# Optimization experiments

Hardware: AMD Instinct MI355X
Metric: run time of the kernel (lower is better)

The kernel has to match this reference:

```python
import jax, jax.numpy as jnp
import numpy as np

NEG_LARGE = -2.0**32 + 1.0


def setup_inputs() -> dict:
    key = jax.random.key(0)
    ks = jax.random.split(key, 8)
    B, L, D = 2048, 200, 64  # D = embedding_dim, features are 2D wide
    H1, H2 = 80, 40
    queries = jax.random.normal(ks[0], (B, 2 * D), dtype=jnp.float32)
    user_behaviors = jax.random.normal(ks[1], (B, L, 2 * D), dtype=jnp.float32)
    masks = jax.random.randint(ks[2], (B, L), 0, 2, dtype=jnp.int32)
    s = 1.0 / np.sqrt(8 * D)
    w1 = jax.random.uniform(ks[3], (8 * D, H1), minval=-s, maxval=s, dtype=jnp.float32)
    b1 = jnp.zeros((H1,), jnp.float32)
    s2 = 1.0 / np.sqrt(H1)
    w2 = jax.random.uniform(ks[4], (H1, H2), minval=-s2, maxval=s2, dtype=jnp.float32)
    b2 = jnp.zeros((H2,), jnp.float32)
    s3 = 1.0 / np.sqrt(H2)
    w3 = jax.random.uniform(ks[5], (H2, 1), minval=-s3, maxval=s3, dtype=jnp.float32)
    b3 = jnp.zeros((1,), jnp.float32)
    return {"queries": queries, "user_behaviors": user_behaviors, "masks": masks,
            "w1": w1, "b1": b1, "w2": w2, "b2": b2, "w3": w3, "b3": b3}


def reference(queries, user_behaviors, masks, w1, b1, w2, b2, w3, b3):
    B, L, twoD = user_behaviors.shape
    q = jnp.broadcast_to(queries[:, None, :], (B, L, twoD))  # (B, L, 2D)
    feats = jnp.concatenate([q, user_behaviors, q - user_behaviors,
                             q * user_behaviors], axis=-1)  # (B, L, 8D)
    h = jax.nn.sigmoid(jnp.einsum('blf,fh->blh', feats, w1) + b1)
    h = jax.nn.sigmoid(jnp.einsum('blh,hk->blk', h, w2) + b2)
    scores = jnp.einsum('blk,ko->blo', h, w3) + b3  # (B, L, 1)
    valid = (masks != 0)[:, :, None]
    scores = jnp.where(valid, scores, NEG_LARGE)
    attn = jax.nn.softmax(scores, axis=1)  # (B, L, 1)
    return jnp.sum(attn * user_behaviors, axis=1)  # (B, 2D)
```

## Files before the change

### kernel.cpp

```cpp
#include <hip/hip_runtime.h>
#include <cstddef>


#define L_   200
#define D2_  128

typedef __attribute__((ext_vector_type(8))) short bf16x8;
typedef __attribute__((ext_vector_type(4))) float f32x4;
typedef __attribute__((ext_vector_type(4))) unsigned int u32x4;

__device__ __forceinline__ float sigmoidf_(float x) { return 1.0f / (1.0f + __expf(-x)); }

__device__ __forceinline__ unsigned int f2bf_(float x) {
  unsigned int u = __float_as_uint(x);
  return (u + 0x7fffu + ((u >> 16) & 1u)) >> 16;
}
__device__ __forceinline__ unsigned int pk2_(float a, float b) {
  return f2bf_(a) | (f2bf_(b) << 16);
}

extern "C" __global__ void __launch_bounds__(256, 3)
din_attn_kernel(const float* __restrict__ queries,
                const float* __restrict__ ub,
                const int*   __restrict__ masks,
                const float* __restrict__ w1,
                const float* __restrict__ b1,
                const float* __restrict__ w2,
                const float* __restrict__ b2,
                const float* __restrict__ w3,
                float* __restrict__ out)
{
  __shared__ __align__(16) char pool[39936];
  __shared__ __align__(16) char w2f[9216];
  __shared__ __align__(16) float q_s[128];
  __shared__ __align__(16) float qt_s[80];
  __shared__ __align__(16) float b2_s[48];
  __shared__ __align__(16) float w3_s[48];
  __shared__ __align__(16) float scores_s[208];
  __shared__ float red_s[8];

  const int b    = blockIdx.x;
  const int t    = threadIdx.x;
  const int wave = t >> 6;
  const int lane = t & 63;

  const float* ubbase = ub + (size_t)b * L_ * D2_;
  const float4* ub4base = (const float4*)ubbase;

  if (t < 128) q_s[t] = queries[(size_t)b * D2_ + t];
  if (t < 48) {
    b2_s[t] = (t < 40) ? b2[t] : 0.0f;
    w3_s[t] = (t < 40) ? w3[t] : 0.0f;
  }
  __syncthreads();

  if (t < 80) {
    float acc = b1[t];
    #pragma unroll 4
    for (int k = 0; k < 128; ++k)
      acc += q_s[k] * (w1[k * 80 + t] + w1[(256 + k) * 80 + t]);
    qt_s[t] = acc;
  }

  {
    u32x4* dst = (u32x4*)(pool + 13312);
    #pragma unroll
    for (int i = 0; i < 5; ++i) {
      int s = i * 256 + t;
      int n = s & 15, kg = (s >> 4) & 3, g = s >> 6;
      int kc = g / 5, nt = g - kc * 5;
      int h = nt * 16 + n, k0 = kc * 32 + kg * 8;
      float wv[8];
      #pragma unroll
      for (int j = 0; j < 8; ++j) {
        int k = k0 + j;
        wv[j] = w1[(128 + k) * 80 + h] - w1[(256 + k) * 80 + h]
              + q_s[k] * w1[(384 + k) * 80 + h];
      }
      u32x4 v = { pk2_(wv[0], wv[1]), pk2_(wv[2], wv[3]),
                  pk2_(wv[4], wv[5]), pk2_(wv[6], wv[7]) };
      dst[s] = v;
    }
  }

  {
    u32x4* dst = (u32x4*)w2f;
    #pragma unroll
    for (int i = 0; i < 3; ++i) {
      int s = i * 256 + t;
      if (s < 576) {
        int n = s & 15, g = s >> 4;
        int nt2 = g / 12, kg = g - nt2 * 12;
        int j = nt2 * 16 + n;
        u32x4 v = { 0u, 0u, 0u, 0u };
        if (j < 40 && kg < 10) {
          int k0 = kg * 8;
          float e0 = w2[(k0 + 0) * 40 + j], e1 = w2[(k0 + 1) * 40 + j];
          float e2 = w2[(k0 + 2) * 40 + j], e3 = w2[(k0 + 3) * 40 + j];
          float e4 = w2[(k0 + 4) * 40 + j], e5 = w2[(k0 + 5) * 40 + j];
          float e6 = w2[(k0 + 6) * 40 + j], e7 = w2[(k0 + 7) * 40 + j];
          v = (u32x4){ pk2_(e0, e1), pk2_(e2, e3), pk2_(e4, e5), pk2_(e6, e7) };
        }
        dst[s] = v;
      }
    }
  }

  f32x4 acc[17];
  #pragma unroll
  for (int i = 0; i < 17; ++i) acc[i] = (f32x4){0.f, 0.f, 0.f, 0.f};

  const bf16x8* Af = (const bf16x8*)pool;
  const bf16x8* Bf = (const bf16x8*)(pool + 13312);

  for (int kc = 0; kc < 4; ++kc) {
    u32x4* dst = (u32x4*)pool;
    #pragma unroll
    for (int i = 0; i < 4; ++i) {
      int s = i * 256 + t;
      if (s < 832) {
        int m = s & 15, kg = (s >> 4) & 3, mt = s >> 6;
        int l = mt * 16 + m;
        u32x4 v = { 0u, 0u, 0u, 0u };
        if (l < L_) {
          const float4* src = (const float4*)(ubbase + (size_t)l * D2_ + kc * 32 + kg * 8);
          float4 u0 = src[0], u1 = src[1];
          v = (u32x4){ pk2_(u0.x, u0.y), pk2_(u0.z, u0.w), pk2_(u1.x, u1.y), pk2_(u1.z, u1.w) };
        }
        dst[s] = v;
      }
    }
    __syncthreads();

    #pragma unroll
    for (int i = 0; i < 17; ++i) {
      int tt = i * 4 + wave;
      if (tt < 65) {
        int mt = tt / 5, nt = tt - mt * 5;
        bf16x8 av = Af[mt * 64 + lane];
        bf16x8 bv = Bf[(kc * 5 + nt) * 64 + lane];
        acc[i] = __builtin_amdgcn_mfma_f32_16x16x32_bf16(av, bv, acc[i], 0, 0, 0);
      }
    }
    __syncthreads();
  }

  {
    u32x4* pz = (u32x4*)pool;
    #pragma unroll
    for (int s = 0; s < 2; ++s) {
      int idx = s * 256 + t;
      if (idx < 416) {
        int mt = idx >> 5, off = idx & 31;
        pz[(mt * 12 + 10) * 16 + off] = (u32x4){ 0u, 0u, 0u, 0u };
      }
    }
    unsigned short* hv = (unsigned short*)pool;
    const int n = lane & 15, rg = lane >> 4;
    #pragma unroll
    for (int i = 0; i < 17; ++i) {
      int tt = i * 4 + wave;
      if (tt < 65) {
        int mt = tt / 5, nt = tt - mt * 5;
        int h = nt * 16 + n;
        int kg = h >> 3, hb = h & 7;
        float qtv = qt_s[h];
        #pragma unroll
        for (int r = 0; r < 4; ++r) {
          float x = acc[i][r] + qtv;
          hv[((mt * 12 + kg) * 16 + rg * 4 + r) * 8 + hb] = (unsigned short)f2bf_(sigmoidf_(x));
        }
      }
    }
  }
  __syncthreads();

  f32x4 acc2[4][3];
  #pragma unroll
  for (int i = 0; i < 4; ++i)
    #pragma unroll
    for (int n2 = 0; n2 < 3; ++n2) acc2[i][n2] = (f32x4){0.f, 0.f, 0.f, 0.f};

  {
    const bf16x8* hvf = (const bf16x8*)pool;
    const bf16x8* w2ff = (const bf16x8*)w2f;
    #pragma unroll
    for (int i = 0; i < 4; ++i) {
      int mt = wave + i * 4;
      if (mt < 13) {
        #pragma unroll
        for (int ks = 0; ks < 3; ++ks) {
          bf16x8 av = hvf[mt * 192 + ks * 64 + lane];
          #pragma unroll
          for (int n2 = 0; n2 < 3; ++n2) {
            bf16x8 bv = w2ff[n2 * 192 + ks * 64 + lane];
            acc2[i][n2] = __builtin_amdgcn_mfma_f32_16x16x32_bf16(av, bv, acc2[i][n2], 0, 0, 0);
          }
        }
      }
    }
  }

  {
    const int n = lane & 15, rg = lane >> 4;
    #pragma unroll
    for (int i = 0; i < 4; ++i) {
      int mt = wave + i * 4;
      if (mt < 13) {
        #pragma unroll
        for (int r = 0; r < 4; ++r) {
          float s = 0.0f;
          #pragma unroll
          for (int n2 = 0; n2 < 3; ++n2) {
            int j = n2 * 16 + n;
            s += sigmoidf_(acc2[i][n2][r] + b2_s[j]) * w3_s[j];
          }
          s += __shfl_xor(s, 1, 64);
          s += __shfl_xor(s, 2, 64);
          s += __shfl_xor(s, 4, 64);
          s += __shfl_xor(s, 8, 64);
          int l = mt * 16 + rg * 4 + r;
          if (n == 0 && l < L_) scores_s[l] = s;
        }
      }
    }
  }
  __syncthreads();

  float sval = -INFINITY;
  if (t < L_) {
    int mv = masks[(size_t)b * L_ + t];
    sval = mv ? scores_s[t] : -4294967295.0f;
  }
  float m = sval;
  #pragma unroll
  for (int o = 32; o > 0; o >>= 1) m = fmaxf(m, __shfl_xor(m, o, 64));
  if (lane == 0) red_s[wave] = m;
  __syncthreads();
  m = fmaxf(fmaxf(red_s[0], red_s[1]), fmaxf(red_s[2], red_s[3]));
  float e = (t < L_) ? __expf(sval - m) : 0.0f;
  float ssum = e;
  #pragma unroll
  for (int o = 32; o > 0; o >>= 1) ssum += __shfl_xor(ssum, o, 64);
  if (lane == 0) red_s[4 + wave] = ssum;
  __syncthreads();
  ssum = red_s[4] + red_s[5] + red_s[6] + red_s[7];
  float attn = e / ssum;
  __syncthreads();
  if (t < L_) scores_s[t] = attn;
  __syncthreads();

  {
    float* wsum = (float*)pool;
    int d4 = t & 31;
    int lg = t >> 5;
    float4 o = make_float4(0.f, 0.f, 0.f, 0.f);
    #pragma unroll 5
    for (int l = lg; l < L_; l += 8) {
      float w = scores_s[l];
      float4 v = ub4base[l * 32 + d4];
      o.x += w * v.x; o.y += w * v.y; o.z += w * v.z; o.w += w * v.w;
    }
    *(float4*)(wsum + lg * 136 + d4 * 4) = o;
    __syncthreads();
    if (t < 128) {
      float s = 0.0f;
      #pragma unroll
      for (int g = 0; g < 8; ++g) s += wsum[g * 136 + t];
      out[(size_t)b * 128 + t] = s;
    }
  }
}

extern "C" void kernel_launch(void* const* d_in, const int* in_sizes, int n_in,
                              void* d_out, int out_size, void* d_ws, size_t ws_size,
                              hipStream_t stream) {
  const float* queries = (const float*)d_in[0];
  const float* ub      = (const float*)d_in[1];
  const int*   masks   = (const int*)d_in[2];
  const float* w1      = (const float*)d_in[3];
  const float* b1      = (const float*)d_in[4];
  const float* w2      = (const float*)d_in[5];
  const float* b2      = (const float*)d_in[6];
  const float* w3      = (const float*)d_in[7];
  float* out = (float*)d_out;

  const int B = in_sizes[0] / D2_;
  din_attn_kernel<<<B, 256, 0, stream>>>(queries, ub, masks, w1, b1, w2, b2, w3, out);
}
```

Baseline: 391.0 us.

## Split weight prep into setup kernel and load MFMA A operands directly from global

Moves the per-batch qt projection and the batch-invariant W1/W2 re-layout into a separate setup kernel that writes to workspace. The main kernel then only combines precomputed wbc + q*wd, and w2 fragments are read from global memory. Behavior rows are now loaded straight into registers as MFMA A operands, so the per-chunk LDS staging and its barriers go away, and the B fragments are kept in registers. Together with the smaller LDS footprint this allows 4 blocks per CU. The cost is an extra kernel launch, uncoalesced per-lane global loads for the A operands, and global reads of w2 fragments.

```diff
diff --git a/kernel.cpp b/kernel.cpp
--- a/kernel.cpp
+++ b/kernel.cpp
@@ -9,6 +9,8 @@
 typedef __attribute__((ext_vector_type(4))) float f32x4;
 typedef __attribute__((ext_vector_type(4))) unsigned int u32x4;
 
+union U8 { u32x4 u; bf16x8 b; };
+
 __device__ __forceinline__ float sigmoidf_(float x) { return 1.0f / (1.0f + __expf(-x)); }
 
 __device__ __forceinline__ unsigned int f2bf_(float x) {
@@ -19,20 +21,89 @@
   return f2bf_(a) | (f2bf_(b) << 16);
 }
 
-extern "C" __global__ void __launch_bounds__(256, 3)
+extern "C" __global__ void __launch_bounds__(128)
+din_setup_kernel(const float* __restrict__ queries,
+                 const float* __restrict__ w1,
+                 const float* __restrict__ b1,
+                 const float* __restrict__ w2,
+                 float* __restrict__ qt,
+                 float* __restrict__ wbc,
+                 float* __restrict__ wd,
+                 u32x4* __restrict__ w2a,
+                 u32x4* __restrict__ w2b)
+{
+  const int bb = blockIdx.x;
+  const int t  = threadIdx.x;
+
+  if (bb < 8) {
+    for (int s = bb * 160 + t; s < bb * 160 + 160; s += 128) {
+      int nn = s & 15, kg = (s >> 4) & 3, g = s >> 6;
+      int kc = g / 5, nt = g - kc * 5;
+      int h = nt * 16 + nn, k0 = kc * 32 + kg * 8;
+      #pragma unroll
+      for (int j = 0; j < 8; ++j) {
+        int k = k0 + j;
+        wbc[s * 8 + j] = w1[(128 + k) * 80 + h] - w1[(256 + k) * 80 + h];
+        wd [s * 8 + j] = w1[(384 + k) * 80 + h];
+      }
+    }
+  } else if (bb == 8) {
+    for (int s = t; s < 384; s += 128) {
+      int nn = s & 15, g = s >> 4, nt2 = g >> 3, kg = g & 7;
+      int j = nt2 * 16 + nn, k0 = kg * 8;
+      u32x4 v = { 0u, 0u, 0u, 0u };
+      if (j < 40) {
+        float e0 = w2[(k0 + 0) * 40 + j], e1 = w2[(k0 + 1) * 40 + j];
+        float e2 = w2[(k0 + 2) * 40 + j], e3 = w2[(k0 + 3) * 40 + j];
+        float e4 = w2[(k0 + 4) * 40 + j], e5 = w2[(k0 + 5) * 40 + j];
+        float e6 = w2[(k0 + 6) * 40 + j], e7 = w2[(k0 + 7) * 40 + j];
+        v = (u32x4){ pk2_(e0, e1), pk2_(e2, e3), pk2_(e4, e5), pk2_(e6, e7) };
+      }
+      w2a[s] = v;
+    }
+    for (int s = t; s < 96; s += 128) {
+      int nn = s & 15, g = s >> 4, nt2 = g >> 1, kgt = g & 1;
+      int j = nt2 * 16 + nn, k0 = 64 + kgt * 8;
+      u32x4 v = { 0u, 0u, 0u, 0u };
+      if (j < 40) {
+        float e0 = w2[(k0 + 0) * 40 + j], e1 = w2[(k0 + 1) * 40 + j];
+        float e2 = w2[(k0 + 2) * 40 + j], e3 = w2[(k0 + 3) * 40 + j];
+        float e4 = w2[(k0 + 4) * 40 + j], e5 = w2[(k0 + 5) * 40 + j];
+        float e6 = w2[(k0 + 6) * 40 + j], e7 = w2[(k0 + 7) * 40 + j];
+        v = (u32x4){ pk2_(e0, e1), pk2_(e2, e3), pk2_(e4, e5), pk2_(e6, e7) };
+      }
+      w2b[s] = v;
+    }
+  } else {
+    const int b = bb - 9;
+    __shared__ float qs[128];
+    if (t < 128) qs[t] = queries[(size_t)b * D2_ + t];
+    __syncthreads();
+    if (t < 80) {
+      float acc = b1[t];
+      #pragma unroll 4
+      for (int k = 0; k < 128; ++k)
+        acc += qs[k] * (w1[k * 80 + t] + w1[(256 + k) * 80 + t]);
+      qt[(size_t)b * 80 + t] = acc;
+    }
+  }
+}
+
+extern "C" __global__ void __launch_bounds__(256, 4)
 din_attn_kernel(const float* __restrict__ queries,
                 const float* __restrict__ ub,
                 const int*   __restrict__ masks,
-                const float* __restrict__ w1,
-                const float* __restrict__ b1,
-                const float* __restrict__ w2,
                 const float* __restrict__ b2,
                 const float* __restrict__ w3,
+                const float* __restrict__ qt,
+                const float* __restrict__ wbc,
+                const float* __restrict__ wd,
+                const u32x4* __restrict__ w2a,
+                const u32x4* __restrict__ w2b,
                 float* __restrict__ out)
 {
-  __shared__ __align__(16) char pool[39936];
-  __shared__ __align__(16) char w2f[9216];
-  __shared__ __align__(16) float q_s[128];
+  __shared__ __align__(16) char  pool[33280];
+  __shared__ __align__(16) float wsum_s[1088];
   __shared__ __align__(16) float qt_s[80];
   __shared__ __align__(16) float b2_s[48];
   __shared__ __align__(16) float w3_s[48];
@@ -43,184 +114,143 @@
   const int t    = threadIdx.x;
   const int wave = t >> 6;
   const int lane = t & 63;
-
-  const float* ubbase = ub + (size_t)b * L_ * D2_;
-  const float4* ub4base = (const float4*)ubbase;
-
-  if (t < 128) q_s[t] = queries[(size_t)b * D2_ + t];
+  const int n16  = lane & 15;
+  const int rg   = lane >> 4;
+
+  const float* ubbase = ub + (size_t)b * (L_ * D2_);
+  const float* qrow   = queries + (size_t)b * D2_;
+
+  if (t < 80) qt_s[t] = qt[(size_t)b * 80 + t];
   if (t < 48) {
     b2_s[t] = (t < 40) ? b2[t] : 0.0f;
     w3_s[t] = (t < 40) ? w3[t] : 0.0f;
   }
-  __syncthreads();
-
-  if (t < 80) {
-    float acc = b1[t];
-    #pragma unroll 4
-    for (int k = 0; k < 128; ++k)
-      acc += q_s[k] * (w1[k * 80 + t] + w1[(256 + k) * 80 + t]);
-    qt_s[t] = acc;
-  }
 
   {
-    u32x4* dst = (u32x4*)(pool + 13312);
+    u32x4* dst = (u32x4*)pool;
+    const float4* wbc4 = (const float4*)wbc;
+    const float4* wd4  = (const float4*)wd;
     #pragma unroll
     for (int i = 0; i < 5; ++i) {
       int s = i * 256 + t;
-      int n = s & 15, kg = (s >> 4) & 3, g = s >> 6;
-      int kc = g / 5, nt = g - kc * 5;
-      int h = nt * 16 + n, k0 = kc * 32 + kg * 8;
-      float wv[8];
-      #pragma unroll
-      for (int j = 0; j < 8; ++j) {
-        int k = k0 + j;
-        wv[j] = w1[(128 + k) * 80 + h] - w1[(256 + k) * 80 + h]
-              + q_s[k] * w1[(384 + k) * 80 + h];
-      }
-      u32x4 v = { pk2_(wv[0], wv[1]), pk2_(wv[2], wv[3]),
-                  pk2_(wv[4], wv[5]), pk2_(wv[6], wv[7]) };
-      dst[s] = v;
-    }
-  }
-
-  {
-    u32x4* dst = (u32x4*)w2f;
-    #pragma unroll
-    for (int i = 0; i < 3; ++i) {
-      int s = i * 256 + t;
-      if (s < 576) {
-        int n = s & 15, g = s >> 4;
-        int nt2 = g / 12, kg = g - nt2 * 12;
-        int j = nt2 * 16 + n;
-        u32x4 v = { 0u, 0u, 0u, 0u };
-        if (j < 40 && kg < 10) {
-          int k0 = kg * 8;
-          float e0 = w2[(k0 + 0) * 40 + j], e1 = w2[(k0 + 1) * 40 + j];
-          float e2 = w2[(k0 + 2) * 40 + j], e3 = w2[(k0 + 3) * 40 + j];
-          float e4 = w2[(k0 + 4) * 40 + j], e5 = w2[(k0 + 5) * 40 + j];
-          float e6 = w2[(k0 + 6) * 40 + j], e7 = w2[(k0 + 7) * 40 + j];
-          v = (u32x4){ pk2_(e0, e1), pk2_(e2, e3), pk2_(e4, e5), pk2_(e6, e7) };
-        }
-        dst[s] = v;
-      }
-    }
-  }
-
-  f32x4 acc[17];
-  #pragma unroll
-  for (int i = 0; i < 17; ++i) acc[i] = (f32x4){0.f, 0.f, 0.f, 0.f};
-
-  const bf16x8* Af = (const bf16x8*)pool;
-  const bf16x8* Bf = (const bf16x8*)(pool + 13312);
-
-  for (int kc = 0; kc < 4; ++kc) {
-    u32x4* dst = (u32x4*)pool;
-    #pragma unroll
-    for (int i = 0; i < 4; ++i) {
-      int s = i * 256 + t;
-      if (s < 832) {
-        int m = s & 15, kg = (s >> 4) & 3, mt = s >> 6;
-        int l = mt * 16 + m;
-        u32x4 v = { 0u, 0u, 0u, 0u };
-        if (l < L_) {
-          const float4* src = (const float4*)(ubbase + (size_t)l * D2_ + kc * 32 + kg * 8);
-          float4 u0 = src[0], u1 = src[1];
-          v = (u32x4){ pk2_(u0.x, u0.y), pk2_(u0.z, u0.w), pk2_(u1.x, u1.y), pk2_(u1.z, u1.w) };
-        }
-        dst[s] = v;
-      }
-    }
-    __syncthreads();
-
-    #pragma unroll
-    for (int i = 0; i < 17; ++i) {
-      int tt = i * 4 + wave;
-      if (tt < 65) {
-        int mt = tt / 5, nt = tt - mt * 5;
-        bf16x8 av = Af[mt * 64 + lane];
-        bf16x8 bv = Bf[(kc * 5 + nt) * 64 + lane];
-        acc[i] = __builtin_amdgcn_mfma_f32_16x16x32_bf16(av, bv, acc[i], 0, 0, 0);
-      }
-    }
-    __syncthreads();
-  }
-
-  {
-    u32x4* pz = (u32x4*)pool;
-    #pragma unroll
-    for (int s = 0; s < 2; ++s) {
-      int idx = s * 256 + t;
-      if (idx < 416) {
-        int mt = idx >> 5, off = idx & 31;
-        pz[(mt * 12 + 10) * 16 + off] = (u32x4){ 0u, 0u, 0u, 0u };
-      }
-    }
-    unsigned short* hv = (unsigned short*)pool;
-    const int n = lane & 15, rg = lane >> 4;
-    #pragma unroll
-    for (int i = 0; i < 17; ++i) {
-      int tt = i * 4 + wave;
-      if (tt < 65) {
-        int mt = tt / 5, nt = tt - mt * 5;
-        int h = nt * 16 + n;
-        int kg = h >> 3, hb = h & 7;
-        float qtv = qt_s[h];
-        #pragma unroll
-        for (int r = 0; r < 4; ++r) {
-          float x = acc[i][r] + qtv;
-          hv[((mt * 12 + kg) * 16 + rg * 4 + r) * 8 + hb] = (unsigned short)f2bf_(sigmoidf_(x));
-        }
-      }
-    }
-  }
-  __syncthreads();
-
-  f32x4 acc2[4][3];
+      int kg = (s >> 4) & 3, g = s >> 6;
+      int kc = g / 5;
+      int k0 = kc * 32 + kg * 8;
+      float4 c0 = wbc4[2 * s], c1 = wbc4[2 * s + 1];
+      float4 d0 = wd4 [2 * s], d1 = wd4 [2 * s + 1];
+      float4 q0 = *(const float4*)(qrow + k0);
+      float4 q1 = *(const float4*)(qrow + k0 + 4);
+      dst[s] = (u32x4){ pk2_(c0.x + q0.x * d0.x, c0.y + q0.y * d0.y),
+                        pk2_(c0.z + q0.z * d0.z, c0.w + q0.w * d0.w),
+                        pk2_(c1.x + q1.x * d1.x, c1.y + q1.y * d1.y),
+                        pk2_(c1.z + q1.z * d1.z, c1.w + q1.w * d1.w) };
+    }
+  }
+  __syncthreads();
+
+  f32x4 acc[4][5];
   #pragma unroll
   for (int i = 0; i < 4; ++i)
     #pragma unroll
-    for (int n2 = 0; n2 < 3; ++n2) acc2[i][n2] = (f32x4){0.f, 0.f, 0.f, 0.f};
-
-  {
-    const bf16x8* hvf = (const bf16x8*)pool;
-    const bf16x8* w2ff = (const bf16x8*)w2f;
+    for (int nt = 0; nt < 5; ++nt) acc[i][nt] = (f32x4){0.f, 0.f, 0.f, 0.f};
+
+  const bf16x8* Bf = (const bf16x8*)pool;
+
+  for (int kc = 0; kc < 4; ++kc) {
+    bf16x8 bvv[5];
+    #pragma unroll
+    for (int nt = 0; nt < 5; ++nt) bvv[nt] = Bf[(kc * 5 + nt) * 64 + lane];
     #pragma unroll
     for (int i = 0; i < 4; ++i) {
       int mt = wave + i * 4;
       if (mt < 13) {
-        #pragma unroll
-        for (int ks = 0; ks < 3; ++ks) {
-          bf16x8 av = hvf[mt * 192 + ks * 64 + lane];
-          #pragma unroll
-          for (int n2 = 0; n2 < 3; ++n2) {
-            bf16x8 bv = w2ff[n2 * 192 + ks * 64 + lane];
-            acc2[i][n2] = __builtin_amdgcn_mfma_f32_16x16x32_bf16(av, bv, acc2[i][n2], 0, 0, 0);
-          }
-        }
-      }
-    }
-  }
+        int row = mt * 16 + n16;
+        float4 u0 = make_float4(0.f, 0.f, 0.f, 0.f);
+        float4 u1 = make_float4(0.f, 0.f, 0.f, 0.f);
+        if (row < L_) {
+          const float4* src = (const float4*)(ubbase + (size_t)row * D2_ + kc * 32 + rg * 8);
+          u0 = src[0]; u1 = src[1];
+        }
+        U8 av;
+        av.u = (u32x4){ pk2_(u0.x, u0.y), pk2_(u0.z, u0.w),
+                        pk2_(u1.x, u1.y), pk2_(u1.z, u1.w) };
+        #pragma unroll
+        for (int nt = 0; nt < 5; ++nt)
+          acc[i][nt] = __builtin_amdgcn_mfma_f32_16x16x32_bf16(av.b, bvv[nt], acc[i][nt], 0, 0, 0);
+      }
+    }
+  }
+  __syncthreads();
 
   {
-    const int n = lane & 15, rg = lane >> 4;
+    unsigned short* hv = (unsigned short*)pool;
     #pragma unroll
     for (int i = 0; i < 4; ++i) {
       int mt = wave + i * 4;
       if (mt < 13) {
+        #pragma unroll
+        for (int nt = 0; nt < 5; ++nt) {
+          int h = nt * 16 + n16;
+          float qtv = qt_s[h];
+          int kg = h >> 3;
+          int slotbase = (kg < 8) ? (mt * 8 + kg) : (1664 + mt * 2 + (kg - 8));
+          #pragma unroll
+          for (int r = 0; r < 4; ++r) {
+            float x = acc[i][nt][r] + qtv;
+            hv[(slotbase * 16 + rg * 4 + r) * 8 + (h & 7)] =
+                (unsigned short)f2bf_(sigmoidf_(x));
+          }
+        }
+      }
+    }
+  }
+
+  {
+    const bf16x8* hvf  = (const bf16x8*)pool;
+    const bf16x8* w2af = (const bf16x8*)w2a;
+    const bf16x8* w2bf = (const bf16x8*)w2b;
+    #pragma unroll
+    for (int i = 0; i < 4; ++i) {
+      int mt = wave + i * 4;
+      if (mt < 13) {
+        f32x4 acc2[3];
+        #pragma unroll
+        for (int n2 = 0; n2 < 3; ++n2) acc2[n2] = (f32x4){0.f, 0.f, 0.f, 0.f};
+
+        #pragma unroll
+        for (int ks = 0; ks < 2; ++ks) {
+          bf16x8 av = hvf[(mt * 8 + ks * 4 + rg) * 16 + n16];
+          #pragma unroll
+          for (int n2 = 0; n2 < 3; ++n2) {
+            bf16x8 bv = w2af[(n2 * 8 + ks * 4 + rg) * 16 + n16];
+            acc2[n2] = __builtin_amdgcn_mfma_f32_16x16x32_bf16(av, bv, acc2[n2], 0, 0, 0);
+          }
+        }
+        {
+          bf16x8 av = (bf16x8){0, 0, 0, 0, 0, 0, 0, 0};
+          if (lane < 32) av = hvf[(1664 + mt * 2 + rg) * 16 + n16];
+          #pragma unroll
+          for (int n2 = 0; n2 < 3; ++n2) {
+            bf16x8 bv = (bf16x8){0, 0, 0, 0, 0, 0, 0, 0};
+            if (lane < 32) bv = w2bf[(n2 * 2 + rg) * 16 + n16];
+            acc2[n2] = __builtin_amdgcn_mfma_f32_16x16x32_bf16(av, bv, acc2[n2], 0, 0, 0);
+          }
+        }
+
         #pragma unroll
         for (int r = 0; r < 4; ++r) {
           float s = 0.0f;
           #pragma unroll
           for (int n2 = 0; n2 < 3; ++n2) {
-            int j = n2 * 16 + n;
-            s += sigmoidf_(acc2[i][n2][r] + b2_s[j]) * w3_s[j];
+            int j = n2 * 16 + n16;
+            s += sigmoidf_(acc2[n2][r] + b2_s[j]) * w3_s[j];
           }
           s += __shfl_xor(s, 1, 64);
           s += __shfl_xor(s, 2, 64);
           s += __shfl_xor(s, 4, 64);
           s += __shfl_xor(s, 8, 64);
           int l = mt * 16 + rg * 4 + r;
-          if (n == 0 && l < L_) scores_s[l] = s;
+          if (n16 == 0 && l < L_) scores_s[l] = s;
         }
       }
     }
@@ -251,7 +281,7 @@
   __syncthreads();
 
   {
-    float* wsum = (float*)pool;
+    const float4* ub4base = (const float4*)ubbase;
     int d4 = t & 31;
     int lg = t >> 5;
     float4 o = make_float4(0.f, 0.f, 0.f, 0.f);
@@ -261,12 +291,12 @@
       float4 v = ub4base[l * 32 + d4];
       o.x += w * v.x; o.y += w * v.y; o.z += w * v.z; o.w += w * v.w;
     }
-    *(float4*)(wsum + lg * 136 + d4 * 4) = o;
+    *(float4*)(wsum_s + lg * 136 + d4 * 4) = o;
     __syncthreads();
     if (t < 128) {
       float s = 0.0f;
       #pragma unroll
-      for (int g = 0; g < 8; ++g) s += wsum[g * 136 + t];
+      for (int g = 0; g < 8; ++g) s += wsum_s[g * 136 + t];
       out[(size_t)b * 128 + t] = s;
     }
   }
@@ -286,5 +316,15 @@
   float* out = (float*)d_out;
 
   const int B = in_sizes[0] / D2_;
-  din_attn_kernel<<<B, 256, 0, stream>>>(queries, ub, masks, w1, b1, w2, b2, w3, out);
-}
+
+  char*  ws  = (char*)d_ws;
+  float* qt  = (float*)ws;
+  float* wbc = (float*)(ws + (size_t)B * 320);
+  float* wd  = (float*)(ws + (size_t)B * 320 + 40960);
+  u32x4* w2a = (u32x4*)(ws + (size_t)B * 320 + 81920);
+  u32x4* w2b = (u32x4*)(ws + (size_t)B * 320 + 88064);
+
+  din_setup_kernel<<<B + 9, 128, 0, stream>>>(queries, w1, b1, w2, qt, wbc, wd, w2a, w2b);
+  din_attn_kernel<<<B, 256, 0, stream>>>(queries, ub, masks, b2, w3,
+                                         qt, wbc, wd, w2a, w2b, out);
+}
```

Result: faster. 358.1 us (-8.4%).
